# Optimization experiments

Hardware: AMD Instinct MI355X
Metric: run time of the kernel (lower is better)

Reference implementation:

```python
import jax, jax.numpy as jnp
import numpy as np

NUM_USERS = 100000
NUM_ITEMS = 50000
N_NODES = NUM_USERS + NUM_ITEMS
LATENT_DIM = 64
N_LAYERS = 3
N_EDGES = 1200000
K = 0.8  # laplace-k blending: Graph = (1-k)*I + k*G


def setup_inputs() -> dict:
    key = jax.random.key(0)
    k1, k2, k3, k4, k5, k6, k7 = jax.random.split(key, 7)
    # xavier_uniform for embeddings: bound = sqrt(6/(fan_in+fan_out))
    bu = float(np.sqrt(6.0 / (NUM_USERS + LATENT_DIM)))
    bi = float(np.sqrt(6.0 / (NUM_ITEMS + LATENT_DIM)))
    user_emb = jax.random.uniform(k1, (NUM_USERS, LATENT_DIM), jnp.float32, -bu, bu)
    item_emb = jax.random.uniform(k2, (NUM_ITEMS, LATENT_DIM), jnp.float32, -bi, bi)
    edge_row = jax.random.randint(k3, (N_EDGES,), 0, N_NODES)
    edge_col = jax.random.randint(k4, (N_EDGES,), 0, N_NODES)
    # normalized-adjacency-like positive values
    edge_val = jax.random.uniform(k5, (N_EDGES,), jnp.float32) * 0.01
    users = jax.random.randint(k6, (4096,), 0, NUM_USERS)
    items = jax.random.randint(k7, (4096,), 0, NUM_ITEMS)
    return {"users": users, "items": items, "edge_row": edge_row,
            "edge_col": edge_col, "edge_val": edge_val,
            "user_emb": user_emb, "item_emb": item_emb}


def _spmm(edge_row, edge_col, edge_val, x):
    # y = G @ x via gather + segment_sum over static edge list
    msgs = edge_val[:, None] * x[edge_col]  # [E, D]
    return jax.ops.segment_sum(msgs, edge_row, num_segments=N_NODES)


def _computer(user_emb, item_emb, edge_row, edge_col, edge_val):
    all_emb = jnp.concatenate([user_emb, item_emb], axis=0)  # [N, D]
    acc = all_emb  # running sum of layer embeddings (mean taken at end)
    emb = all_emb
    for _ in range(N_LAYERS):
        # Graph = (1-K)*I + K*G, so spmm(Graph, emb) = (1-K)*emb + K*G@emb
        emb = (1.0 - K) * emb + K * _spmm(edge_row, edge_col, edge_val, emb)
        acc = acc + emb
    light_out = acc / (N_LAYERS + 1)  # mean over stacked layer embeddings
    return light_out[:NUM_USERS], light_out[NUM_USERS:]


def reference(users, items, edge_row, edge_col, edge_val, user_emb, item_emb):
    all_users, all_items = _computer(user_emb, item_emb, edge_row, edge_col, edge_val)
    u = all_users[users]  # [B, D]
    i = all_items[items]  # [B, D]
    gamma = jnp.sum(u * i, axis=1)  # [B]
    return gamma
```

## Files before the change

### kernel.cpp

```cpp
#include <hip/hip_runtime.h>
#include <hip/hip_fp16.h>
#include <stdint.h>
#include <string.h>


#define NUM_USERS 100000
#define NUM_ITEMS 50000
#define N_NODES   150000
#define DIM       64
#define N_EDGES   1200000
#define ND        (N_NODES * DIM)
#define NB        4096
#define NSAMP     (2 * NB)

#define ELL_W     24
#define NBKT      640
#define RPB       235
#define NROWS_PAD (NBKT * RPB)
#define BCAP      2176
#define SCAP      11
#define OVF_CAP   512

#define K1_THREADS     1024
#define K1_EDGE_BLOCKS 256
#define K1_ROUNDS      2
#define K1_MARK_BLOCKS 8
#define K1_CVT_BLOCKS  128

#define S1_ACC_BLOCKS  512
#define S1_EXP_BLOCKS  2048
#define S1_CPY_BLOCKS  586

#define SPMM_BLOCKS    9375
#define ACC_BLOCKS     512

__device__ __forceinline__ int h2i(__half2 h) { int r; memcpy(&r, &h, 4); return r; }
__device__ __forceinline__ __half2 i2h(int i) { __half2 h; memcpy(&h, &i, 4); return h; }

__device__ __forceinline__ float4 loadh4(const __half* p) {
    int2 v = *(const int2*)p;
    float2 a = __half22float2(i2h(v.x));
    float2 b = __half22float2(i2h(v.y));
    return make_float4(a.x, a.y, b.x, b.y);
}
__device__ __forceinline__ void storeh4(__half* p, float4 v) {
    int2 o;
    o.x = h2i(__floats2half2_rn(v.x, v.y));
    o.y = h2i(__floats2half2_rn(v.z, v.w));
    *(int2*)p = o;
}
__device__ __forceinline__ float4 f4fma(float v, float4 x, float4 a) {
    a.x += v * x.x; a.y += v * x.y; a.z += v * x.z; a.w += v * x.w;
    return a;
}

__global__ __launch_bounds__(K1_THREADS)
void k1_kernel(const int* __restrict__ erow,
               const int* __restrict__ ecol,
               const float* __restrict__ evalv,
               const int* __restrict__ users,
               const int* __restrict__ items,
               const float* __restrict__ ue,
               const float* __restrict__ ie,
               int* __restrict__ gtails,
               int2* __restrict__ barr,
               int4* __restrict__ ovf,
               int* __restrict__ ovf_cnt,
               unsigned char* __restrict__ mask3,
               __half* __restrict__ xh) {
    __shared__ int2 stage[NBKT * SCAP];
    __shared__ int  scnt[NBKT];
    if (blockIdx.x < K1_EDGE_BLOCKS) {
        for (int k = threadIdx.x; k < NBKT; k += K1_THREADS) scnt[k] = 0;
        __syncthreads();
        for (int rnd = 0; rnd < K1_ROUNDS; ++rnd) {
            int base = ((rnd * K1_EDGE_BLOCKS + (int)blockIdx.x) * K1_THREADS
                        + (int)threadIdx.x) * 4;
            if (base < N_EDGES) {
                int4   r4 = *(const int4*)(erow + base);
                int4   c4 = *(const int4*)(ecol + base);
                float4 v4 = *(const float4*)(evalv + base);
                int   rr[4] = {r4.x, r4.y, r4.z, r4.w};
                int   cc[4] = {c4.x, c4.y, c4.z, c4.w};
                float vv[4] = {v4.x, v4.y, v4.z, v4.w};
                #pragma unroll
                for (int u = 0; u < 4; ++u) {
                    int b    = rr[u] / RPB;
                    int rloc = rr[u] - b * RPB;
                    int2 rec = make_int2(cc[u] | (rloc << 18), __float_as_int(vv[u]));
                    int s = atomicAdd(&scnt[b], 1);
                    if (s < SCAP) {
                        stage[b * SCAP + s] = rec;
                    } else {
                        atomicSub(&scnt[b], 1);
                        int gp = atomicAdd(&gtails[b], 1);
                        if (gp < BCAP) barr[(size_t)b * BCAP + gp] = rec;
                        else { int q = atomicAdd(ovf_cnt, 1);
                               if (q < OVF_CAP)
                                   ovf[q] = make_int4(rr[u], cc[u], __float_as_int(vv[u]), 0); }
                    }
                }
            }
            __syncthreads();
            for (int b = threadIdx.x; b < NBKT; b += K1_THREADS) {
                int c = scnt[b];
                if (c >= 8) {
                    int gp = atomicAdd(&gtails[b], 8);
                    if (gp + 8 <= BCAP) {
                        int2* dst = barr + (size_t)b * BCAP + gp;
                        #pragma unroll
                        for (int i = 0; i < 8; ++i) dst[i] = stage[b * SCAP + i];
                    } else {
                        for (int i = 0; i < 8; ++i) {
                            int2 rc = stage[b * SCAP + i];
                            if (gp + i < BCAP) barr[(size_t)b * BCAP + gp + i] = rc;
                            else { int q = atomicAdd(ovf_cnt, 1);
                                   if (q < OVF_CAP)
                                       ovf[q] = make_int4(b * RPB + (rc.x >> 18),
                                                          rc.x & 0x3FFFF, rc.y, 0); }
                        }
                    }
                    c -= 8;
                    for (int i = 0; i < c; ++i)
                        stage[b * SCAP + i] = stage[b * SCAP + 8 + i];
                    scnt[b] = c;
                }
            }
            __syncthreads();
        }
        for (int b = threadIdx.x; b < NBKT; b += K1_THREADS) {
            int c = scnt[b];
            if (c > 0) {
                int gp = atomicAdd(&gtails[b], c);
                for (int i = 0; i < c; ++i) {
                    int2 rc = stage[b * SCAP + i];
                    if (gp + i < BCAP) barr[(size_t)b * BCAP + gp + i] = rc;
                    else { int q = atomicAdd(ovf_cnt, 1);
                           if (q < OVF_CAP)
                               ovf[q] = make_int4(b * RPB + (rc.x >> 18),
                                                  rc.x & 0x3FFFF, rc.y, 0); }
                }
            }
        }
    } else if (blockIdx.x < K1_EDGE_BLOCKS + K1_MARK_BLOCKS) {
        int i = ((int)blockIdx.x - K1_EDGE_BLOCKS) * K1_THREADS + (int)threadIdx.x;
        if (i < NB)         mask3[users[i]] = 1;
        else if (i < NSAMP) mask3[NUM_USERS + items[i - NB]] = 1;
    } else {
        const int n4  = ND / 4;
        const int nu4 = NUM_USERS * DIM / 4;
        int i = ((int)blockIdx.x - K1_EDGE_BLOCKS - K1_MARK_BLOCKS) * K1_THREADS
                + (int)threadIdx.x;
        const int stride = K1_CVT_BLOCKS * K1_THREADS;
        int2* xh4 = (int2*)xh;
        for (; i < n4; i += stride) {
            float4 v = (i < nu4) ? ((const float4*)ue)[i]
                                 : ((const float4*)ie)[i - nu4];
            int2 o;
            o.x = h2i(__floats2half2_rn(v.x, v.y));
            o.y = h2i(__floats2half2_rn(v.z, v.w));
            xh4[i] = o;
        }
    }
}

__global__ __launch_bounds__(256)
void s1_kernel(const int* __restrict__ erow,
               const int* __restrict__ ecol,
               const int* __restrict__ gtails,
               const int2* __restrict__ barr,
               const __half* __restrict__ xh,
               const float* __restrict__ ue,
               const float* __restrict__ ie,
               int* __restrict__ counts,
               int2* __restrict__ ell,
               int4* __restrict__ ovf,
               int* __restrict__ ovf_cnt,
               const unsigned char* __restrict__ mask3,
               unsigned char* __restrict__ mask2,
               const int* __restrict__ users,
               const int* __restrict__ items,
               float* __restrict__ acc_small,
               __half* __restrict__ emb_out) {
    __shared__ __align__(16) int2 lell[RPB * ELL_W];
    __shared__ int lcnt[RPB];
    const int wid  = threadIdx.x >> 6;
    const int lane = threadIdx.x & 63;
    const int g    = lane >> 4;
    const int t    = lane & 15;

    if (blockIdx.x < NBKT) {
        const int bkt   = blockIdx.x;
        const int rbase = bkt * RPB;
        for (int k = threadIdx.x; k < RPB; k += 256) lcnt[k] = 0;
        __syncthreads();
        int n = gtails[bkt];
        n = n < BCAP ? n : BCAP;
        for (int e = threadIdx.x; e < n; e += 256) {
            int2 rec = barr[(size_t)bkt * BCAP + e];
            int col  = rec.x & 0x3FFFF;
            int rloc = rec.x >> 18;
            int slot = atomicAdd(&lcnt[rloc], 1);
            if (slot < ELL_W)
                lell[rloc * ELL_W + slot] = make_int2(col, rec.y);
            else { int q = atomicAdd(ovf_cnt, 1);
                   if (q < OVF_CAP) ovf[q] = make_int4(rbase + rloc, col, rec.y, 0); }
        }
        __syncthreads();
        {
            int4* g4 = (int4*)(ell + (size_t)rbase * ELL_W);
            const int4* l4 = (const int4*)lell;
            for (int k = threadIdx.x; k < RPB * ELL_W / 2; k += 256) g4[k] = l4[k];
            for (int k = threadIdx.x; k < RPB; k += 256) counts[rbase + k] = lcnt[k];
        }
        int novf = *ovf_cnt;
        novf = novf < OVF_CAP ? novf : OVF_CAP;
        for (int k = 0; k < 15; ++k) {
            int rloc = wid * 4 + g + 16 * k;
            if (rloc >= RPB) break;
            int row = rbase + rloc;
            if (row >= N_NODES) continue;
            int cnt = lcnt[rloc];
            cnt = cnt < ELL_W ? cnt : ELL_W;
            const int2* ep = &lell[rloc * ELL_W];
            float4 a0 = {0,0,0,0}, a1 = {0,0,0,0}, a2 = {0,0,0,0}, a3 = {0,0,0,0};
            int j = 0;
            for (; j + 4 <= cnt; j += 4) {
                int4 cv0 = *(const int4*)(ep + j);
                int4 cv1 = *(const int4*)(ep + j + 2);
                float4 x0 = loadh4(xh + (size_t)cv0.x * DIM + t * 4);
                float4 x1 = loadh4(xh + (size_t)cv0.z * DIM + t * 4);
                float4 x2 = loadh4(xh + (size_t)cv1.x * DIM + t * 4);
                float4 x3 = loadh4(xh + (size_t)cv1.z * DIM + t * 4);
                a0 = f4fma(__int_as_float(cv0.y), x0, a0);
                a1 = f4fma(__int_as_float(cv0.w), x1, a1);
                a2 = f4fma(__int_as_float(cv1.y), x2, a2);
                a3 = f4fma(__int_as_float(cv1.w), x3, a3);
            }
            for (; j + 2 <= cnt; j += 2) {
                int4 cv = *(const int4*)(ep + j);
                float4 x0 = loadh4(xh + (size_t)cv.x * DIM + t * 4);
                float4 x1 = loadh4(xh + (size_t)cv.z * DIM + t * 4);
                a0 = f4fma(__int_as_float(cv.y), x0, a0);
                a1 = f4fma(__int_as_float(cv.w), x1, a1);
            }
            if (j < cnt) {
                int2 cv = ep[j];
                float4 xv = loadh4(xh + (size_t)cv.x * DIM + t * 4);
                a0 = f4fma(__int_as_float(cv.y), xv, a0);
            }
            for (int q = 0; q < novf; ++q) {
                int4 o = ovf[q];
                if (o.x == row) {
                    float4 xv = loadh4(xh + (size_t)o.y * DIM + t * 4);
                    a0 = f4fma(__int_as_float(o.z), xv, a0);
                }
            }
            float4 self = loadh4(xh + (size_t)row * DIM + t * 4);
            float4 r;
            r.x = 0.2f * self.x + 0.8f * ((a0.x + a1.x) + (a2.x + a3.x));
            r.y = 0.2f * self.y + 0.8f * ((a0.y + a1.y) + (a2.y + a3.y));
            r.z = 0.2f * self.z + 0.8f * ((a0.z + a1.z) + (a2.z + a3.z));
            r.w = 0.2f * self.w + 0.8f * ((a0.w + a1.w) + (a2.w + a3.w));
            storeh4(emb_out + (size_t)row * DIM + t * 4, r);
        }
    } else if (blockIdx.x < NBKT + S1_ACC_BLOCKS) {
        const int s = ((int)blockIdx.x - NBKT) * 16 + wid * 4 + g;
        const int node = (s < NB) ? users[s] : (NUM_USERS + items[s - NB]);
        const float* p = (node < NUM_USERS) ? ue + (size_t)node * DIM
                                            : ie + (size_t)(node - NUM_USERS) * DIM;
        *(float4*)(acc_small + (size_t)s * DIM + t * 4) = *(const float4*)(p + t * 4);
    } else if (blockIdx.x < NBKT + S1_ACC_BLOCKS + S1_EXP_BLOCKS) {
        int i = ((int)blockIdx.x - NBKT - S1_ACC_BLOCKS) * 256 + (int)threadIdx.x;
        const int stride = S1_EXP_BLOCKS * 256;
        for (; i < N_EDGES; i += stride)
            if (mask3[erow[i]]) mask2[ecol[i]] = 1;
    } else {
        int i = ((int)blockIdx.x - NBKT - S1_ACC_BLOCKS - S1_EXP_BLOCKS) * 256
                + (int)threadIdx.x;
        if (i < N_NODES && mask3[i]) mask2[i] = 1;
    }
}

template<bool ACC_STORE>
__global__ void spmm_kernel(const int* __restrict__ counts,
                            const int2* __restrict__ ell,
                            const __half* __restrict__ xsrc,
                            const unsigned char* __restrict__ mask,
                            const int* __restrict__ ovf_cnt,
                            const int4* __restrict__ ovf,
                            const int* __restrict__ users,
                            const int* __restrict__ items,
                            float* __restrict__ acc_small,
                            __half* __restrict__ xout) {
    const int wid  = threadIdx.x >> 6;
    const int lane = threadIdx.x & 63;
    const int g    = lane >> 4;
    const int t    = lane & 15;

    if (blockIdx.x < SPMM_BLOCKS) {
        const int row = blockIdx.x * 16 + wid * 4 + g;
        bool active = mask[row] != 0;
        int cnt = 0;
        if (active) {
            cnt = counts[row];
            cnt = cnt < ELL_W ? cnt : ELL_W;
        }
        const int2* ep = ell + (size_t)row * ELL_W;
        float4 a0 = {0,0,0,0}, a1 = {0,0,0,0}, a2 = {0,0,0,0}, a3 = {0,0,0,0};
        int j = 0;
        for (; j + 4 <= cnt; j += 4) {
            int4 cv0 = *(const int4*)(ep + j);
            int4 cv1 = *(const int4*)(ep + j + 2);
            float4 x0 = loadh4(xsrc + (size_t)cv0.x * DIM + t * 4);
            float4 x1 = loadh4(xsrc + (size_t)cv0.z * DIM + t * 4);
            float4 x2 = loadh4(xsrc + (size_t)cv1.x * DIM + t * 4);
            float4 x3 = loadh4(xsrc + (size_t)cv1.z * DIM + t * 4);
            a0 = f4fma(__int_as_float(cv0.y), x0, a0);
            a1 = f4fma(__int_as_float(cv0.w), x1, a1);
            a2 = f4fma(__int_as_float(cv1.y), x2, a2);
            a3 = f4fma(__int_as_float(cv1.w), x3, a3);
        }
        for (; j + 2 <= cnt; j += 2) {
            int4 cv = *(const int4*)(ep + j);
            float4 x0 = loadh4(xsrc + (size_t)cv.x * DIM + t * 4);
            float4 x1 = loadh4(xsrc + (size_t)cv.z * DIM + t * 4);
            a0 = f4fma(__int_as_float(cv.y), x0, a0);
            a1 = f4fma(__int_as_float(cv.w), x1, a1);
        }
        if (j < cnt) {
            int2 cv = ep[j];
            float4 xv = loadh4(xsrc + (size_t)cv.x * DIM + t * 4);
            a0 = f4fma(__int_as_float(cv.y), xv, a0);
        }
        int novf = *ovf_cnt;
        if (novf > 0) {
            novf = novf < OVF_CAP ? novf : OVF_CAP;
            for (int k = 0; k < novf; ++k) {
                int4 o = ovf[k];
                if (active && o.x == row) {
                    float4 xv = loadh4(xsrc + (size_t)o.y * DIM + t * 4);
                    a0 = f4fma(__int_as_float(o.z), xv, a0);
                }
            }
        }
        if (active) {
            float4 self = loadh4(xsrc + (size_t)row * DIM + t * 4);
            float4 r;
            r.x = 0.2f * self.x + 0.8f * ((a0.x + a1.x) + (a2.x + a3.x));
            r.y = 0.2f * self.y + 0.8f * ((a0.y + a1.y) + (a2.y + a3.y));
            r.z = 0.2f * self.z + 0.8f * ((a0.z + a1.z) + (a2.z + a3.z));
            r.w = 0.2f * self.w + 0.8f * ((a0.w + a1.w) + (a2.w + a3.w));
            storeh4(xout + (size_t)row * DIM + t * 4, r);
        }
    } else {
        const int s = (blockIdx.x - SPMM_BLOCKS) * 16 + wid * 4 + g;
        const int node = (s < NB) ? users[s] : (NUM_USERS + items[s - NB]);
        float4 v = loadh4(xsrc + (size_t)node * DIM + t * 4);
        float4* ap = (float4*)(acc_small + (size_t)s * DIM + t * 4);
        float4 a = *ap;
        a.x += v.x; a.y += v.y; a.z += v.z; a.w += v.w;
        *ap = a;
        (void)ACC_STORE;
    }
}

__global__ void dot_kernel(const int* __restrict__ users,
                           const int* __restrict__ items,
                           const float* __restrict__ acc_small,
                           const __half* __restrict__ emb3,
                           float* __restrict__ out) {
    int w = (blockIdx.x * blockDim.x + threadIdx.x) >> 6;
    int lane = threadIdx.x & 63;
    if (w >= NB) return;
    int u  = users[w];
    int it = items[w];
    float au = acc_small[w * DIM + lane]
             + __half2float(emb3[(size_t)u * DIM + lane]);
    float ai = acc_small[(NB + w) * DIM + lane]
             + __half2float(emb3[(size_t)(NUM_USERS + it) * DIM + lane]);
    float p = au * ai;
    #pragma unroll
    for (int o = 32; o > 0; o >>= 1) p += __shfl_down(p, o, 64);
    if (lane == 0) out[w] = p * (1.0f / 16.0f);
}

extern "C" void kernel_launch(void* const* d_in, const int* in_sizes, int n_in,
                              void* d_out, int out_size, void* d_ws, size_t ws_size,
                              hipStream_t stream) {
    const int*   users = (const int*)  d_in[0];
    const int*   items = (const int*)  d_in[1];
    const int*   erow  = (const int*)  d_in[2];
    const int*   ecol  = (const int*)  d_in[3];
    const float* evalv = (const float*)d_in[4];
    const float* ue    = (const float*)d_in[5];
    const float* ie    = (const float*)d_in[6];
    float* out = (float*)d_out;

    __half* xh        = (__half*)d_ws;
    __half* emb_a     = xh + ND;
    __half* emb_b     = emb_a + ND;
    float*  acc_small = (float*)(emb_b + ND);
    int2*   barr      = (int2*)(acc_small + NSAMP * DIM);
    int2*   ell       = barr + (size_t)NBKT * BCAP;
    int*    counts    = (int*)(ell + (size_t)NROWS_PAD * ELL_W);
    int*    gtails    = counts + NROWS_PAD;
    int*    ovf_cnt   = gtails + NBKT;
    int4*   ovf       = (int4*)(((uintptr_t)(ovf_cnt + 1) + 15) & ~(uintptr_t)15);
    unsigned char* mask3 = (unsigned char*)(ovf + OVF_CAP);
    unsigned char* mask2 = mask3 + N_NODES;

    size_t zbytes = (size_t)((mask2 + N_NODES) - (unsigned char*)gtails);
    hipMemsetAsync(gtails, 0, zbytes, stream);

    k1_kernel<<<K1_EDGE_BLOCKS + K1_MARK_BLOCKS + K1_CVT_BLOCKS, K1_THREADS, 0, stream>>>(
        erow, ecol, evalv, users, items, ue, ie,
        gtails, barr, ovf, ovf_cnt, mask3, xh);

    s1_kernel<<<NBKT + S1_ACC_BLOCKS + S1_EXP_BLOCKS + S1_CPY_BLOCKS, 256, 0, stream>>>(
        erow, ecol, gtails, barr, xh, ue, ie, counts, ell, ovf, ovf_cnt,
        mask3, mask2, users, items, acc_small, emb_a);

    spmm_kernel<false><<<SPMM_BLOCKS + ACC_BLOCKS, 256, 0, stream>>>(
        counts, ell, emb_a, mask2, ovf_cnt, ovf,
        users, items, acc_small, emb_b);

    spmm_kernel<false><<<SPMM_BLOCKS + ACC_BLOCKS, 256, 0, stream>>>(
        counts, ell, emb_b, mask3, ovf_cnt, ovf,
        users, items, acc_small, emb_a);

    dot_kernel<<<(NB * 64 + 255) / 256, 256, 0, stream>>>(
        users, items, acc_small, emb_a, out);
}
```

Measured before the change: 212.0 us.

## Compute final layer only at sampled nodes and write ELL only for needed rows

The final propagation layer is replaced by a small kernel that computes the layer-3 embedding only for the 8192 sampled user/item nodes and adds it directly into the accumulator, so the dot kernel needs no more gathers. The sample mask is built in a tiny pre-kernel, and the two-hop mask expansion moves into the edge-bucketing kernel. ELL rows and counts are now written only for rows in mask2, which cuts global writes. The cost is an extra launch and a per-edge mask lookup during bucketing. The final kernel also folds in the identity term and the previous-layer sum, writing 1.2*self (the 0.2 from (1-K)*I plus 1.0 for the running sum).

```diff
diff --git a/kernel.cpp b/kernel.cpp
--- a/kernel.cpp
+++ b/kernel.cpp
@@ -24,15 +24,12 @@
 #define K1_THREADS     1024
 #define K1_EDGE_BLOCKS 256
 #define K1_ROUNDS      2
-#define K1_MARK_BLOCKS 8
 #define K1_CVT_BLOCKS  128
 
 #define S1_ACC_BLOCKS  512
-#define S1_EXP_BLOCKS  2048
-#define S1_CPY_BLOCKS  586
-
 #define SPMM_BLOCKS    9375
 #define ACC_BLOCKS     512
+#define SP3_BLOCKS     512
 
 __device__ __forceinline__ int h2i(__half2 h) { int r; memcpy(&r, &h, 4); return r; }
 __device__ __forceinline__ __half2 i2h(int i) { __half2 h; memcpy(&h, &i, 4); return h; }
@@ -54,19 +51,29 @@
     return a;
 }
 
+__global__ void k0_kernel(const int* __restrict__ users,
+                          const int* __restrict__ items,
+                          unsigned char* __restrict__ mask3,
+                          unsigned char* __restrict__ mask2) {
+    int i = blockIdx.x * blockDim.x + threadIdx.x;
+    int n = -1;
+    if (i < NB)          n = users[i];
+    else if (i < NSAMP)  n = NUM_USERS + items[i - NB];
+    if (n >= 0) { mask3[n] = 1; mask2[n] = 1; }
+}
+
 __global__ __launch_bounds__(K1_THREADS)
 void k1_kernel(const int* __restrict__ erow,
                const int* __restrict__ ecol,
                const float* __restrict__ evalv,
-               const int* __restrict__ users,
-               const int* __restrict__ items,
                const float* __restrict__ ue,
                const float* __restrict__ ie,
                int* __restrict__ gtails,
                int2* __restrict__ barr,
                int4* __restrict__ ovf,
                int* __restrict__ ovf_cnt,
-               unsigned char* __restrict__ mask3,
+               const unsigned char* __restrict__ mask3,
+               unsigned char* __restrict__ mask2,
                __half* __restrict__ xh) {
     __shared__ int2 stage[NBKT * SCAP];
     __shared__ int  scnt[NBKT];
@@ -85,6 +92,7 @@
                 float vv[4] = {v4.x, v4.y, v4.z, v4.w};
                 #pragma unroll
                 for (int u = 0; u < 4; ++u) {
+                    if (mask3[rr[u]]) mask2[cc[u]] = 1;
                     int b    = rr[u] / RPB;
                     int rloc = rr[u] - b * RPB;
                     int2 rec = make_int2(cc[u] | (rloc << 18), __float_as_int(vv[u]));
@@ -142,15 +150,10 @@
                 }
             }
         }
-    } else if (blockIdx.x < K1_EDGE_BLOCKS + K1_MARK_BLOCKS) {
-        int i = ((int)blockIdx.x - K1_EDGE_BLOCKS) * K1_THREADS + (int)threadIdx.x;
-        if (i < NB)         mask3[users[i]] = 1;
-        else if (i < NSAMP) mask3[NUM_USERS + items[i - NB]] = 1;
     } else {
         const int n4  = ND / 4;
         const int nu4 = NUM_USERS * DIM / 4;
-        int i = ((int)blockIdx.x - K1_EDGE_BLOCKS - K1_MARK_BLOCKS) * K1_THREADS
-                + (int)threadIdx.x;
+        int i = ((int)blockIdx.x - K1_EDGE_BLOCKS) * K1_THREADS + (int)threadIdx.x;
         const int stride = K1_CVT_BLOCKS * K1_THREADS;
         int2* xh4 = (int2*)xh;
         for (; i < n4; i += stride) {
@@ -165,9 +168,7 @@
 }
 
 __global__ __launch_bounds__(256)
-void s1_kernel(const int* __restrict__ erow,
-               const int* __restrict__ ecol,
-               const int* __restrict__ gtails,
+void s1_kernel(const int* __restrict__ gtails,
                const int2* __restrict__ barr,
                const __half* __restrict__ xh,
                const float* __restrict__ ue,
@@ -176,8 +177,7 @@
                int2* __restrict__ ell,
                int4* __restrict__ ovf,
                int* __restrict__ ovf_cnt,
-               const unsigned char* __restrict__ mask3,
-               unsigned char* __restrict__ mask2,
+               const unsigned char* __restrict__ mask2,
                const int* __restrict__ users,
                const int* __restrict__ items,
                float* __restrict__ acc_small,
@@ -210,8 +210,13 @@
         {
             int4* g4 = (int4*)(ell + (size_t)rbase * ELL_W);
             const int4* l4 = (const int4*)lell;
-            for (int k = threadIdx.x; k < RPB * ELL_W / 2; k += 256) g4[k] = l4[k];
-            for (int k = threadIdx.x; k < RPB; k += 256) counts[rbase + k] = lcnt[k];
+            for (int idx = threadIdx.x; idx < RPB * (ELL_W / 2); idx += 256) {
+                int row = idx / (ELL_W / 2);
+                if (rbase + row < N_NODES && mask2[rbase + row]) g4[idx] = l4[idx];
+            }
+            for (int k = threadIdx.x; k < RPB; k += 256)
+                if (rbase + k < N_NODES && mask2[rbase + k])
+                    counts[rbase + k] = lcnt[k];
         }
         int novf = *ovf_cnt;
         novf = novf < OVF_CAP ? novf : OVF_CAP;
@@ -264,25 +269,15 @@
             r.w = 0.2f * self.w + 0.8f * ((a0.w + a1.w) + (a2.w + a3.w));
             storeh4(emb_out + (size_t)row * DIM + t * 4, r);
         }
-    } else if (blockIdx.x < NBKT + S1_ACC_BLOCKS) {
+    } else {
         const int s = ((int)blockIdx.x - NBKT) * 16 + wid * 4 + g;
         const int node = (s < NB) ? users[s] : (NUM_USERS + items[s - NB]);
         const float* p = (node < NUM_USERS) ? ue + (size_t)node * DIM
                                             : ie + (size_t)(node - NUM_USERS) * DIM;
         *(float4*)(acc_small + (size_t)s * DIM + t * 4) = *(const float4*)(p + t * 4);
-    } else if (blockIdx.x < NBKT + S1_ACC_BLOCKS + S1_EXP_BLOCKS) {
-        int i = ((int)blockIdx.x - NBKT - S1_ACC_BLOCKS) * 256 + (int)threadIdx.x;
-        const int stride = S1_EXP_BLOCKS * 256;
-        for (; i < N_EDGES; i += stride)
-            if (mask3[erow[i]]) mask2[ecol[i]] = 1;
-    } else {
-        int i = ((int)blockIdx.x - NBKT - S1_ACC_BLOCKS - S1_EXP_BLOCKS) * 256
-                + (int)threadIdx.x;
-        if (i < N_NODES && mask3[i]) mask2[i] = 1;
-    }
-}
-
-template<bool ACC_STORE>
+    }
+}
+
 __global__ void spmm_kernel(const int* __restrict__ counts,
                             const int2* __restrict__ ell,
                             const __half* __restrict__ xsrc,
@@ -361,25 +356,81 @@
         float4 a = *ap;
         a.x += v.x; a.y += v.y; a.z += v.z; a.w += v.w;
         *ap = a;
-        (void)ACC_STORE;
-    }
-}
-
-__global__ void dot_kernel(const int* __restrict__ users,
+    }
+}
+
+__global__ void sp3_kernel(const int* __restrict__ counts,
+                           const int2* __restrict__ ell,
+                           const __half* __restrict__ emb2,
+                           const int* __restrict__ ovf_cnt,
+                           const int4* __restrict__ ovf,
+                           const int* __restrict__ users,
                            const int* __restrict__ items,
-                           const float* __restrict__ acc_small,
-                           const __half* __restrict__ emb3,
+                           float* __restrict__ acc_small) {
+    const int wid  = threadIdx.x >> 6;
+    const int lane = threadIdx.x & 63;
+    const int g    = lane >> 4;
+    const int t    = lane & 15;
+    const int s = blockIdx.x * 16 + wid * 4 + g;
+    if (s >= NSAMP) return;
+    const int node = (s < NB) ? users[s] : (NUM_USERS + items[s - NB]);
+
+    int cnt = counts[node];
+    cnt = cnt < ELL_W ? cnt : ELL_W;
+    const int2* ep = ell + (size_t)node * ELL_W;
+    float4 a0 = {0,0,0,0}, a1 = {0,0,0,0}, a2 = {0,0,0,0}, a3 = {0,0,0,0};
+    int j = 0;
+    for (; j + 4 <= cnt; j += 4) {
+        int4 cv0 = *(const int4*)(ep + j);
+        int4 cv1 = *(const int4*)(ep + j + 2);
+        float4 x0 = loadh4(emb2 + (size_t)cv0.x * DIM + t * 4);
+        float4 x1 = loadh4(emb2 + (size_t)cv0.z * DIM + t * 4);
+        float4 x2 = loadh4(emb2 + (size_t)cv1.x * DIM + t * 4);
+        float4 x3 = loadh4(emb2 + (size_t)cv1.z * DIM + t * 4);
+        a0 = f4fma(__int_as_float(cv0.y), x0, a0);
+        a1 = f4fma(__int_as_float(cv0.w), x1, a1);
+        a2 = f4fma(__int_as_float(cv1.y), x2, a2);
+        a3 = f4fma(__int_as_float(cv1.w), x3, a3);
+    }
+    for (; j + 2 <= cnt; j += 2) {
+        int4 cv = *(const int4*)(ep + j);
+        float4 x0 = loadh4(emb2 + (size_t)cv.x * DIM + t * 4);
+        float4 x1 = loadh4(emb2 + (size_t)cv.z * DIM + t * 4);
+        a0 = f4fma(__int_as_float(cv.y), x0, a0);
+        a1 = f4fma(__int_as_float(cv.w), x1, a1);
+    }
+    if (j < cnt) {
+        int2 cv = ep[j];
+        float4 xv = loadh4(emb2 + (size_t)cv.x * DIM + t * 4);
+        a0 = f4fma(__int_as_float(cv.y), xv, a0);
+    }
+    int novf = *ovf_cnt;
+    if (novf > 0) {
+        novf = novf < OVF_CAP ? novf : OVF_CAP;
+        for (int k = 0; k < novf; ++k) {
+            int4 o = ovf[k];
+            if (o.x == node) {
+                float4 xv = loadh4(emb2 + (size_t)o.y * DIM + t * 4);
+                a0 = f4fma(__int_as_float(o.z), xv, a0);
+            }
+        }
+    }
+    float4 self = loadh4(emb2 + (size_t)node * DIM + t * 4);
+    float4* ap = (float4*)(acc_small + (size_t)s * DIM + t * 4);
+    float4 a = *ap;
+    a.x += 1.2f * self.x + 0.8f * ((a0.x + a1.x) + (a2.x + a3.x));
+    a.y += 1.2f * self.y + 0.8f * ((a0.y + a1.y) + (a2.y + a3.y));
+    a.z += 1.2f * self.z + 0.8f * ((a0.z + a1.z) + (a2.z + a3.z));
+    a.w += 1.2f * self.w + 0.8f * ((a0.w + a1.w) + (a2.w + a3.w));
+    *ap = a;
+}
+
+__global__ void dot_kernel(const float* __restrict__ acc_small,
                            float* __restrict__ out) {
     int w = (blockIdx.x * blockDim.x + threadIdx.x) >> 6;
     int lane = threadIdx.x & 63;
     if (w >= NB) return;
-    int u  = users[w];
-    int it = items[w];
-    float au = acc_small[w * DIM + lane]
-             + __half2float(emb3[(size_t)u * DIM + lane]);
-    float ai = acc_small[(NB + w) * DIM + lane]
-             + __half2float(emb3[(size_t)(NUM_USERS + it) * DIM + lane]);
-    float p = au * ai;
+    float p = acc_small[w * DIM + lane] * acc_small[(NB + w) * DIM + lane];
     #pragma unroll
     for (int o = 32; o > 0; o >>= 1) p += __shfl_down(p, o, 64);
     if (lane == 0) out[w] = p * (1.0f / 16.0f);
@@ -413,22 +464,21 @@
     size_t zbytes = (size_t)((mask2 + N_NODES) - (unsigned char*)gtails);
     hipMemsetAsync(gtails, 0, zbytes, stream);
 
-    k1_kernel<<<K1_EDGE_BLOCKS + K1_MARK_BLOCKS + K1_CVT_BLOCKS, K1_THREADS, 0, stream>>>(
-        erow, ecol, evalv, users, items, ue, ie,
-        gtails, barr, ovf, ovf_cnt, mask3, xh);
-
-    s1_kernel<<<NBKT + S1_ACC_BLOCKS + S1_EXP_BLOCKS + S1_CPY_BLOCKS, 256, 0, stream>>>(
-        erow, ecol, gtails, barr, xh, ue, ie, counts, ell, ovf, ovf_cnt,
-        mask3, mask2, users, items, acc_small, emb_a);
-
-    spmm_kernel<false><<<SPMM_BLOCKS + ACC_BLOCKS, 256, 0, stream>>>(
+    k0_kernel<<<(NSAMP + 255) / 256, 256, 0, stream>>>(users, items, mask3, mask2);
+
+    k1_kernel<<<K1_EDGE_BLOCKS + K1_CVT_BLOCKS, K1_THREADS, 0, stream>>>(
+        erow, ecol, evalv, ue, ie, gtails, barr, ovf, ovf_cnt, mask3, mask2, xh);
+
+    s1_kernel<<<NBKT + S1_ACC_BLOCKS, 256, 0, stream>>>(
+        gtails, barr, xh, ue, ie, counts, ell, ovf, ovf_cnt, mask2,
+        users, items, acc_small, emb_a);
+
+    spmm_kernel<<<SPMM_BLOCKS + ACC_BLOCKS, 256, 0, stream>>>(
         counts, ell, emb_a, mask2, ovf_cnt, ovf,
         users, items, acc_small, emb_b);
 
-    spmm_kernel<false><<<SPMM_BLOCKS + ACC_BLOCKS, 256, 0, stream>>>(
-        counts, ell, emb_b, mask3, ovf_cnt, ovf,
-        users, items, acc_small, emb_a);
-
-    dot_kernel<<<(NB * 64 + 255) / 256, 256, 0, stream>>>(
-        users, items, acc_small, emb_a, out);
-}
+    sp3_kernel<<<SP3_BLOCKS, 256, 0, stream>>>(
+        counts, ell, emb_b, ovf_cnt, ovf, users, items, acc_small);
+
+    dot_kernel<<<(NB * 64 + 255) / 256, 256, 0, stream>>>(acc_small, out);
+}
```

New measurement: 223.0 us. 1.05x slower.
